# Performance work log

Measured on AMD Instinct MI355X. Metric: run time of the kernel, lower is better.

The kernel has to match this reference:

```python
import jax, jax.numpy as jnp
import numpy as np

ALPHA = 0.9

def setup_inputs() -> dict:
    key = jax.random.key(0)
    inputs = jax.random.normal(key, (16, 4000, 512), dtype=jnp.float32)
    return {"inputs": inputs}

def reference(inputs) -> jnp.ndarray:
    # y_t = (1-alpha) * y_{t-1} + alpha * x_t, with y_{-1} = 0
    # (matches torch loop: y_0 = alpha * x_0)
    a = jnp.asarray(ALPHA, dtype=inputs.dtype)
    one_minus_a = jnp.asarray(1.0 - ALPHA, dtype=inputs.dtype)
    x_t = jnp.swapaxes(inputs, 0, 1)  # [T, B, C] for scan over time

    def step(carry, x):
        y = one_minus_a * carry + a * x
        return y, y

    init = jnp.zeros(x_t.shape[1:], dtype=inputs.dtype)  # [B, C]
    _, ys = jax.lax.scan(step, init, x_t)  # ys: [T, B, C]
    return jnp.swapaxes(ys, 0, 1)  # [B, T, C]
```

## Files before the change

### kernel.cpp

```cpp
#include <hip/hip_runtime.h>


constexpr int B_ = 16;
constexpr int T_ = 4000;
constexpr int C_ = 512;
constexpr int L_ = 16;
constexpr int W_ = 8;
constexpr int NC4_ = C_ / 4;
constexpr int NCHUNK_ = T_ / L_;
constexpr int NXCD_ = 8;
constexpr int NWG_ = B_ * NC4_ * NCHUNK_ / 256;
constexpr int CPX_ = NWG_ / NXCD_;

__global__ __launch_bounds__(256, 4) void ema_chunk_scan(const float* __restrict__ x,
                                                         float* __restrict__ y) {
    int swz = (blockIdx.x % NXCD_) * CPX_ + blockIdx.x / NXCD_;

    int half = threadIdx.x >> 7;
    int c4   = threadIdx.x & (NC4_ - 1);
    int b     = swz / 125;
    int chunk = (swz % 125) * 2 + half;

    int t0 = chunk * L_;
    int tw = (chunk > 0) ? (t0 - W_) : 0;

    const float4* base = (const float4*)(x + (size_t)b * T_ * C_) + c4;
    float4*       q    = (float4*)(y + ((size_t)b * T_ + t0) * C_) + c4;

    float4 w[W_];
    #pragma unroll
    for (int i = 0; i < W_; ++i) w[i] = base[(size_t)(tw + i) * NC4_];
    float4 m[L_];
    #pragma unroll
    for (int i = 0; i < L_; ++i) m[i] = base[(size_t)(t0 + i) * NC4_];
    __builtin_amdgcn_sched_barrier(0);

    const float a = 0.9f, om = 0.1f;
    float4 acc = make_float4(0.f, 0.f, 0.f, 0.f);

    #pragma unroll
    for (int i = 0; i < W_; ++i) {
        acc.x = om * acc.x + a * w[i].x;
        acc.y = om * acc.y + a * w[i].y;
        acc.z = om * acc.z + a * w[i].z;
        acc.w = om * acc.w + a * w[i].w;
    }
    float sel = (chunk > 0) ? 1.f : 0.f;
    acc.x *= sel; acc.y *= sel; acc.z *= sel; acc.w *= sel;

    float4 o[L_];
    #pragma unroll
    for (int i = 0; i < L_; ++i) {
        acc.x = om * acc.x + a * m[i].x;
        acc.y = om * acc.y + a * m[i].y;
        acc.z = om * acc.z + a * m[i].z;
        acc.w = om * acc.w + a * m[i].w;
        o[i] = acc;
    }
    __builtin_amdgcn_sched_barrier(0);

    #pragma unroll
    for (int i = 0; i < L_; ++i) {
        q[(size_t)i * NC4_] = o[i];
    }
}

extern "C" void kernel_launch(void* const* d_in, const int* in_sizes, int n_in,
                              void* d_out, int out_size, void* d_ws, size_t ws_size,
                              hipStream_t stream) {
    const float* x = (const float*)d_in[0];
    float* y = (float*)d_out;
    ema_chunk_scan<<<NWG_, 256, 0, stream>>>(x, y);
}
```

Before: 229.9 us.

## Use long per-workgroup time segments with double-buffered streaming loads

Each workgroup now scans a 125-step time segment for all 128 float4 channel columns of one batch, replacing the earlier 16-step chunks. Because every segment still needs an 8-step warmup read, longer segments cut the redundant warmup traffic from half the chunk length to a small fraction. Loads are streamed in 5-row phases through two ping-pong register buffers, so the next phase's loads overlap the current phase's recurrence and stores. The cost is a much smaller grid (512 workgroups of 128 threads), which lowers occupancy and the memory parallelism available to hide latency.

```diff
diff --git a/kernel.cpp b/kernel.cpp
--- a/kernel.cpp
+++ b/kernel.cpp
@@ -1,67 +1,73 @@
 #include <hip/hip_runtime.h>
 
 
-constexpr int B_ = 16;
-constexpr int T_ = 4000;
-constexpr int C_ = 512;
-constexpr int L_ = 16;
-constexpr int W_ = 8;
+constexpr int B_   = 16;
+constexpr int T_   = 4000;
+constexpr int C_   = 512;
 constexpr int NC4_ = C_ / 4;
-constexpr int NCHUNK_ = T_ / L_;
+constexpr int V_   = 125;
+constexpr int NSEG_ = T_ / V_;
+constexpr int W_   = 8;
+constexpr int PH_  = 5;
+constexpr int NPH_ = V_ / PH_;
 constexpr int NXCD_ = 8;
-constexpr int NWG_ = B_ * NC4_ * NCHUNK_ / 256;
-constexpr int CPX_ = NWG_ / NXCD_;
+constexpr int NWG_  = B_ * NSEG_;
+constexpr int CPX_  = NWG_ / NXCD_;
 
-__global__ __launch_bounds__(256, 4) void ema_chunk_scan(const float* __restrict__ x,
-                                                         float* __restrict__ y) {
-    int swz = (blockIdx.x % NXCD_) * CPX_ + blockIdx.x / NXCD_;
-
-    int half = threadIdx.x >> 7;
-    int c4   = threadIdx.x & (NC4_ - 1);
-    int b     = swz / 125;
-    int chunk = (swz % 125) * 2 + half;
-
-    int t0 = chunk * L_;
-    int tw = (chunk > 0) ? (t0 - W_) : 0;
+__global__ __launch_bounds__(128, 2) void ema_seg_scan(const float* __restrict__ x,
+                                                       float* __restrict__ y) {
+    int swz = (blockIdx.x & (NXCD_ - 1)) * CPX_ + blockIdx.x / NXCD_;
+    int c4  = threadIdx.x;
+    int b   = swz >> 5;
+    int seg = swz & (NSEG_ - 1);
+    int t0  = seg * V_;
 
     const float4* base = (const float4*)(x + (size_t)b * T_ * C_) + c4;
     float4*       q    = (float4*)(y + ((size_t)b * T_ + t0) * C_) + c4;
 
-    float4 w[W_];
-    #pragma unroll
-    for (int i = 0; i < W_; ++i) w[i] = base[(size_t)(tw + i) * NC4_];
-    float4 m[L_];
-    #pragma unroll
-    for (int i = 0; i < L_; ++i) m[i] = base[(size_t)(t0 + i) * NC4_];
-    __builtin_amdgcn_sched_barrier(0);
+    const float a = 0.9f, om = 0.1f;
+    auto fma4 = [&](float4& acc, const float4& v) {
+        acc.x = om * acc.x + a * v.x;
+        acc.y = om * acc.y + a * v.y;
+        acc.z = om * acc.z + a * v.z;
+        acc.w = om * acc.w + a * v.w;
+    };
 
-    const float a = 0.9f, om = 0.1f;
     float4 acc = make_float4(0.f, 0.f, 0.f, 0.f);
 
+    {
+        int tw = (seg > 0) ? (t0 - W_) : 0;
+        float4 w[W_];
+        #pragma unroll
+        for (int i = 0; i < W_; ++i) w[i] = base[(size_t)(tw + i) * NC4_];
+        #pragma unroll
+        for (int i = 0; i < W_; ++i) fma4(acc, w[i]);
+        float sel = (seg > 0) ? 1.f : 0.f;
+        acc.x *= sel; acc.y *= sel; acc.z *= sel; acc.w *= sel;
+    }
+
+    float4 bufA[PH_], bufB[PH_];
     #pragma unroll
-    for (int i = 0; i < W_; ++i) {
-        acc.x = om * acc.x + a * w[i].x;
-        acc.y = om * acc.y + a * w[i].y;
-        acc.z = om * acc.z + a * w[i].z;
-        acc.w = om * acc.w + a * w[i].w;
-    }
-    float sel = (chunk > 0) ? 1.f : 0.f;
-    acc.x *= sel; acc.y *= sel; acc.z *= sel; acc.w *= sel;
-
-    float4 o[L_];
-    #pragma unroll
-    for (int i = 0; i < L_; ++i) {
-        acc.x = om * acc.x + a * m[i].x;
-        acc.y = om * acc.y + a * m[i].y;
-        acc.z = om * acc.z + a * m[i].z;
-        acc.w = om * acc.w + a * m[i].w;
-        o[i] = acc;
-    }
-    __builtin_amdgcn_sched_barrier(0);
+    for (int i = 0; i < PH_; ++i) bufA[i] = base[(size_t)(t0 + i) * NC4_];
 
     #pragma unroll
-    for (int i = 0; i < L_; ++i) {
-        q[(size_t)i * NC4_] = o[i];
+    for (int p = 0; p < (NPH_ - 1) / 2; ++p) {
+        const int rA = (2 * p) * PH_;
+        const int rB = (2 * p + 1) * PH_;
+        const int rC = (2 * p + 2) * PH_;
+        #pragma unroll
+        for (int i = 0; i < PH_; ++i) bufB[i] = base[(size_t)(t0 + rB + i) * NC4_];
+        #pragma unroll
+        for (int i = 0; i < PH_; ++i) { fma4(acc, bufA[i]); q[(size_t)(rA + i) * NC4_] = acc; }
+        #pragma unroll
+        for (int i = 0; i < PH_; ++i) bufA[i] = base[(size_t)(t0 + rC + i) * NC4_];
+        #pragma unroll
+        for (int i = 0; i < PH_; ++i) { fma4(acc, bufB[i]); q[(size_t)(rB + i) * NC4_] = acc; }
+    }
+    #pragma unroll
+    for (int i = 0; i < PH_; ++i) {
+        fma4(acc, bufA[i]);
+        q[(size_t)(V_ - PH_ + i) * NC4_] = acc;
     }
 }
 
@@ -70,5 +76,5 @@
                               hipStream_t stream) {
     const float* x = (const float*)d_in[0];
     float* y = (float*)d_out;
-    ema_chunk_scan<<<NWG_, 256, 0, stream>>>(x, y);
+    ema_seg_scan<<<NWG_, 128, 0, stream>>>(x, y);
 }
```

New measurement: 235.2 us. 1.02x slower.
